# Optimization experiments

Hardware: AMD Instinct MI355X
Metric: run time of the kernel (lower is better)

The kernel has to match this reference:

```python
import jax, jax.numpy as jnp
import numpy as np

N, E = 32768, 262144
IN_C, OUT_C = 128, 128
N_GRAPHS = 64


def setup_inputs() -> dict:
    key = jax.random.key(0)
    ks = jax.random.split(key, 8)
    x = jax.random.normal(ks[0], (N, IN_C), dtype=jnp.float32)
    edge_index = jax.random.randint(ks[1], (2, E), 0, N, dtype=jnp.int32)
    batch = jnp.sort(jax.random.randint(ks[2], (N,), 0, N_GRAPHS, dtype=jnp.int32))
    rand = jax.random.uniform(ks[3], (E,), dtype=jnp.float32)  # replaces random.random() draws
    lim_t = 1.0 / np.sqrt(IN_C)
    W_t = jax.random.uniform(ks[4], (IN_C, OUT_C), jnp.float32, -lim_t, lim_t)
    b_t = jax.random.uniform(ks[5], (OUT_C,), jnp.float32, -lim_t, lim_t)
    lim_s = 1.0 / np.sqrt(OUT_C)
    W_s = jax.random.uniform(ks[6], (OUT_C, 1), jnp.float32, -lim_s, lim_s)
    b_s = jax.random.uniform(ks[7], (1,), jnp.float32, -lim_s, lim_s)
    return dict(x=x, edge_index=edge_index, batch=batch, rand=rand,
                W_t=W_t, b_t=b_t, W_s=W_s, b_s=b_s)


def _greedy_match(scores, src, dst, rand, n):
    """Sequential greedy edge matching over score-sorted edges.
    Returns (order, cid_sorted, n_merged): cid_sorted[i] is the cluster id
    assigned to sorted edge i, or -1 if rejected/skipped."""
    scores = jax.lax.stop_gradient(scores)  # indices are non-differentiable (torch uses .item())
    rand = jax.lax.stop_gradient(rand)
    order = jnp.argsort(-scores)
    s_o, d_o = src[order], dst[order]
    acc = rand[order] <= scores[order]  # torch: skip edge if r > edge_score

    def step(carry, inp):
        avail, nxt = carry
        s, t, a = inp
        ok = a & avail[s] & avail[t]
        cid = jnp.where(ok, nxt, -1)
        avail = avail.at[s].set(avail[s] & ~ok)
        avail = avail.at[t].set(avail[t] & ~ok)
        return (avail, nxt + ok.astype(jnp.int32)), cid

    (_, n_merged), cid_sorted = jax.lax.scan(
        step, (jnp.ones((n,), bool), jnp.int32(0)), (s_o, d_o, acc))
    return order, cid_sorted, n_merged


def reference(x, edge_index, batch, rand, W_t, b_t, W_s, b_s):
    n = x.shape[0]
    src, dst = edge_index[0], edge_index[1]
    # merge_edge_sum + transform (eval mode, dropout p=0)
    x_merged = (x[src] + x[dst]) @ W_t + b_t          # [E, OUT_C]
    x_self = (x + x) @ W_t + b_t                      # [N, OUT_C] (self-edge merge)
    e = jax.nn.sigmoid((x_merged @ W_s).reshape(-1) + b_s[0])  # [E] edge scores

    order, cid_sorted, n_merged = _greedy_match(e, src, dst, rand, n)
    ok = cid_sorted >= 0                              # accepted sorted edges
    s_o, d_o = src[order], dst[order]

    # node -> cluster assignment (sentinel index n is dropped)
    cluster = jnp.full((n,), -1, jnp.int32)
    cluster = cluster.at[jnp.where(ok, s_o, n)].set(cid_sorted, mode='drop')
    cluster = cluster.at[jnp.where(ok, d_o, n)].set(cid_sorted, mode='drop')
    remaining = cluster < 0
    rem_rank = jnp.cumsum(remaining.astype(jnp.int32)) - 1  # ascending node order, like set iteration
    cluster = jnp.where(remaining, n_merged + rem_rank, cluster)
    num_clusters = n_merged + remaining.sum().astype(jnp.int32)

    # pooled features, padded to [n, OUT_C]; rows [0, num_clusters) are valid
    mcid = jnp.where(ok, cid_sorted, n)
    new_x = jnp.zeros((n, x_merged.shape[1]), x.dtype)
    new_x = new_x.at[mcid].set(x_merged[order], mode='drop')
    new_x = new_x.at[jnp.where(remaining, cluster, n)].set(x_self, mode='drop')

    # per-cluster edge score (1.0 for unmerged singleton nodes)
    new_edge_score = jnp.ones((n,), e.dtype).at[mcid].set(e[order], mode='drop')

    # new batch vector: new_batch[cluster[v]] = batch[v]
    new_batch = jnp.zeros((n,), batch.dtype).at[cluster].set(batch)

    # remapped edges + coalesce/remove_self_loops expressed as a validity mask
    new_ei = cluster[edge_index]                      # [2, E]
    key = new_ei[0].astype(jnp.int64) * n + new_ei[1].astype(jnp.int64)
    perm = jnp.argsort(key)
    ksorted = key[perm]
    first = jnp.concatenate([jnp.array([True]), ksorted[1:] != ksorted[:-1]])
    unique = jnp.zeros((key.shape[0],), bool).at[perm].set(first)
    edge_valid = unique & (new_ei[0] != new_ei[1])

    return new_x, cluster, new_batch, new_edge_score, num_clusters, new_ei, edge_valid, e
```

## Files before the change

### kernel.cpp

```cpp
#include <hip/hip_runtime.h>
#include <stdint.h>

typedef unsigned int u32;
typedef unsigned long long u64;

#define NN 32768
#define NE 262144
#define NC 128

#define O0 0u
#define O1 4194304u
#define O2 4227072u
#define O3 4259840u
#define O4 4292608u
#define O5 4292609u
#define O6 4816897u
#define O7 5079041u

#define HCAP (1u<<19)
#define NFULL 8
#define CNT0 8
#define MCAP 16384
#define SCAP 32768
#define SNB 32
#define MAXK 0xFFFFFFFFFFFFFFFFull
#define PREFLAG (1ull<<62)

__global__ void ep_init(const float* Wt, const float* Ws, const float* bt, const float* bs,
                        double* u, double* c0, u32* counters,
                        u64* b0, u64* b1, u32* avail, int* cl,
                        u32* tkey, u32* tmin) {
    u32 i = blockIdx.x*blockDim.x + threadIdx.x;
    if (blockIdx.x == 0 && threadIdx.x < 128) {
        int r = threadIdx.x;
        double s = 0.0;
        for (int j = 0; j < NC; j++) s += (double)Wt[r*NC+j] * (double)Ws[j];
        u[r] = s;
        if (r == 0) {
            double c = 0.0;
            for (int j = 0; j < NC; j++) c += (double)bt[j] * (double)Ws[j];
            *c0 = c + (double)bs[0];
        }
    }
    if (i < 64) counters[i] = 0u;
    if (i < NN) { b0[i] = MAXK; b1[i] = MAXK; cl[i] = -1; }
    if (i < NN/32) avail[i] = 0xFFFFFFFFu;
    for (u32 j = i; j < HCAP; j += 131072u) { tkey[j] = 0xFFFFFFFFu; tmin[j] = 0xFFFFFFFFu; }
}

__global__ void ep_ynode(const float* x, const double* u, double* y) {
    int gid = blockIdx.x*blockDim.x + threadIdx.x;
    int v = gid >> 6, lane = threadIdx.x & 63;
    if (v >= NN) return;
    double t = (double)x[v*NC+lane]*u[lane] + (double)x[v*NC+lane+64]*u[lane+64];
    for (int off = 32; off; off >>= 1) t += __shfl_down(t, off, 64);
    if (lane == 0) y[v] = t;
}

__global__ void ep_escore(const int* src, const int* dst, const float* rnd, const double* y,
                          const double* c0, u64* fkey, u64* fdat, u32* counters, float* out) {
    int e = blockIdx.x*blockDim.x + threadIdx.x;
    if (e >= NE) return;
    int s = src[e], d = dst[e];
    double z = y[s] + y[d] + *c0;
    double sc = 1.0/(1.0 + exp(-z));
    out[O7 + e] = (float)sc;
    u64 b = (u64)__double_as_longlong(z);
    u64 ord = (b & 0x8000000000000000ull) ? ~b : (b | 0x8000000000000000ull);
    u64 P = ((~ord) & 0xFFFFFFFFFFFC0000ull) | (u64)(u32)e;
    if ((double)rnd[e] <= sc) {
        u32 p = atomicAdd(&counters[CNT0], 1u);
        fkey[p] = P;
        fdat[p] = ((u64)(u32)e << 30) | ((u64)(u32)s << 15) | (u64)(u32)d;
    }
}

__device__ __forceinline__ bool ep_bit(const u32* a, u32 v) { return (a[v>>5] >> (v&31)) & 1u; }

__global__ void ep_rA(const u64* fkey, const u64* fdat, const u32* cnt, u64* bt, const u32* avail) {
    u32 n = *cnt;
    for (u32 i = blockIdx.x*blockDim.x + threadIdx.x; i < n; i += 131072u) {
        u64 v = fdat[i];
        u32 s = (u32)((v>>15)&0x7FFF), d = (u32)(v&0x7FFF);
        if (ep_bit(avail, s) && ep_bit(avail, d)) {
            u64 P = fkey[i];
            atomicMin(&bt[s], P); atomicMin(&bt[d], P);
        }
    }
}

__global__ void ep_rB(const u64* fkey, const u64* fdat, const u32* cnt, u32* cntN,
                      u64* fkeyN, u64* fdatN, const u64* bt, u64* btN, u32* avail,
                      u64* mkey, u64* mpay, u32* counters) {
    u32 n = *cnt;
    for (u32 i = blockIdx.x*blockDim.x + threadIdx.x; i < n; i += 131072u) {
        u64 v = fdat[i];
        u32 s = (u32)((v>>15)&0x7FFF), d = (u32)(v&0x7FFF);
        if (!ep_bit(avail, s) || !ep_bit(avail, d)) continue;
        u64 P = fkey[i];
        if (bt[s] == P && bt[d] == P) {
            u32 slot = atomicAdd(&counters[2], 1u);
            mkey[slot] = P; mpay[slot] = v;
            atomicAnd(&avail[s>>5], ~(1u<<(s&31)));
            atomicAnd(&avail[d>>5], ~(1u<<(d&31)));
        } else {
            u32 p = atomicAdd(cntN, 1u);
            fkeyN[p] = P; fdatN[p] = v;
            btN[s] = MAXK; btN[d] = MAXK;
        }
    }
}

__global__ void ep_merge(const u64* mk, const u64* mp, const u64* fk, const u64* fd,
                         u32* counters, u64* ck, u64* cd2) {
    u32 i = blockIdx.x*blockDim.x + threadIdx.x;
    u32 nm0 = counters[2];
    u32 cr  = counters[CNT0+NFULL];
    if (i == 0) { u32 tot = nm0 + cr; counters[4] = tot > SCAP ? SCAP : tot; }
    u64 K = MAXK, D = 0;
    if (i < nm0) { K = mk[i]; D = mp[i] | PREFLAG; }
    else if (i < nm0 + cr && i < SCAP) { K = fk[i-nm0]; D = fd[i-nm0]; }
    ck[i] = K; cd2[i] = D;
}

__global__ void ms_hist(const u64* key, u32* hist, int shift) {
    __shared__ u32 h[256];
    int t = threadIdx.x;
    for (int i = t; i < 256; i += 64) h[i] = 0;
    __syncthreads();
    int base = blockIdx.x*1024 + t*16;
    for (int j = 0; j < 16; j++) {
        u32 dg = (u32)(key[base+j] >> shift) & 255u;
        atomicAdd(&h[dg], 1u);
    }
    __syncthreads();
    for (int i = t; i < 256; i += 64) hist[i*SNB + blockIdx.x] = h[i];
}

__global__ void ms_scan(u32* hist) {
    int t = threadIdx.x;
    int per = 256*SNB/64;
    int base = t*per;
    u32 s = 0;
    for (int j = 0; j < per; j++) s += hist[base+j];
    u32 x = s;
    for (int off = 1; off < 64; off <<= 1) { u32 yv = __shfl_up(x, off, 64); if (t >= off) x += yv; }
    u32 run = x - s;
    for (int j = 0; j < per; j++) { u32 tmp = hist[base+j]; hist[base+j] = run; run += tmp; }
}

__global__ void ms_scat(const u64* ki, const u64* pi, u64* ko, u64* po, const u32* hist, int shift) {
    __shared__ unsigned short m[256][64];
    int t = threadIdx.x;
    for (int i = t; i < 256*32; i += 64) ((u32*)m)[i] = 0u;
    __syncthreads();
    int base = blockIdx.x*1024 + t*16;
    u64 kr[16]; u32 dg[16];
    #pragma unroll
    for (int j = 0; j < 16; j++) {
        kr[j] = ki[base+j];
        dg[j] = (u32)(kr[j] >> shift) & 255u;
        m[dg[j]][t]++;
    }
    __syncthreads();
    for (int k = 0; k < 4; k++) {
        int d = t*4 + k;
        u32 run = 0;
        for (int tt = 0; tt < 64; tt++) { u32 tmp = m[d][tt]; m[d][tt] = (unsigned short)run; run += tmp; }
    }
    __syncthreads();
    #pragma unroll
    for (int j = 0; j < 16; j++) {
        u32 d = dg[j];
        u32 pos = hist[d*SNB + blockIdx.x] + m[d][t];
        m[d][t]++;
        ko[pos] = kr[j];
        po[pos] = pi[base+j];
    }
}

__global__ void ep_csum(const u64* sd, const u32* counters, u32* mflag, u32* csums) {
    u32 i = blockIdx.x*1024 + threadIdx.x;
    u32 cnt = counters[4];
    u64 v = sd[i];
    bool pre = (i < cnt) && ((v & PREFLAG) != 0);
    bool cand = (i < cnt) && !pre;
    mflag[i] = pre ? 1u : 0u;
    int c = __syncthreads_count(cand ? 1 : 0);
    if (threadIdx.x == 0) csums[blockIdx.x] = (u32)c;
}

__global__ void ep_cscan(u32* csums, u32* counters, int which) {
    int t = threadIdx.x;
    u32 v = (t < SNB) ? csums[t] : 0u;
    u32 x = v;
    for (int off = 1; off < 64; off <<= 1) { u32 y = __shfl_up(x, off, 64); if (t >= off) x += y; }
    if (t < SNB) csums[t] = x - v;
    if (t == SNB-1) counters[which] = x;
}

__global__ void ep_cemit(const u64* sd, const u32* counters, const u32* csums, u32* candIdx) {
    __shared__ u32 w[16];
    int t = threadIdx.x;
    u32 i = blockIdx.x*1024 + t;
    u32 cnt = counters[4];
    u64 v = sd[i];
    bool pre = (i < cnt) && ((v & PREFLAG) != 0);
    u32 c = ((i < cnt) && !pre) ? 1u : 0u;
    u32 x = c;
    for (int off = 1; off < 64; off <<= 1) { u32 y = __shfl_up(x, off, 64); if ((t&63) >= off) x += y; }
    if ((t&63) == 63) w[t>>6] = x;
    __syncthreads();
    if (t < 16) {
        u32 ww = w[t];
        for (int off = 1; off < 16; off <<= 1) { u32 y = __shfl_up(ww, off, 16); if (t >= off) ww += y; }
        w[t] = ww;
    }
    __syncthreads();
    u32 excl = ((t>>6) ? w[(t>>6)-1] : 0u) + x - c;
    if (c) candIdx[csums[blockIdx.x] + excl] = i;
}

__global__ void __launch_bounds__(1024) ep_walk(const u64* sd, const u32* candIdx,
                                                const u32* counters, const u32* availG,
                                                u32* mflag) {
    __shared__ u32 avail[1024];
    __shared__ u32 claim[16384];
    int t = threadIdx.x;
    avail[t] = availG[t];
    for (int j = t; j < 16384; j += 1024) claim[j] = 0xFFFFFFFFu;
    __syncthreads();
    u32 ncand = counters[5];
    for (u32 base = 0; base < ncand; base += 1024) {
        u32 j = base + t;
        bool have = j < ncand;
        u32 i = 0, s = 0, d = 0;
        if (have) {
            i = candIdx[j];
            u64 v = sd[i];
            s = (u32)((v>>15)&0x7FFF); d = (u32)(v&0x7FFF);
        }
        int st;
        if (!have) st = 1;
        else st = (((avail[s>>5]>>(s&31))&1u) && ((avail[d>>5]>>(d&31))&1u)) ? 0 : 1;
        for (int it = 0; __syncthreads_count(st == 0) > 0 && it < 300; it++) {
            u32 hs = s & 16383u, hd = d & 16383u;
            bool wrote = false;
            if (st == 0) { atomicMin(&claim[hs], (u32)t); atomicMin(&claim[hd], (u32)t); wrote = true; }
            __syncthreads();
            if (st == 0 && claim[hs] == (u32)t && claim[hd] == (u32)t) {
                st = 2;
                atomicAnd(&avail[s>>5], ~(1u<<(s&31)));
                atomicAnd(&avail[d>>5], ~(1u<<(d&31)));
            }
            __syncthreads();
            if (wrote) { claim[hs] = 0xFFFFFFFFu; claim[hd] = 0xFFFFFFFFu; }
            if (st == 0) {
                if (!((avail[s>>5]>>(s&31))&1u) || !((avail[d>>5]>>(d&31))&1u)) st = 1;
            }
        }
        if (st == 2) mflag[i] = 1u;
        __syncthreads();
    }
}

__global__ void ep_msum(const u32* mflag, u32* msums) {
    u32 i = blockIdx.x*1024 + threadIdx.x;
    int c = __syncthreads_count(mflag[i] != 0 ? 1 : 0);
    if (threadIdx.x == 0) msums[blockIdx.x] = (u32)c;
}

__global__ void ep_memit(const u64* sd, const u32* mflag, const u32* msums,
                         const int* batch, u64* Mlist, int* cl, float* out) {
    __shared__ u32 w[16];
    int t = threadIdx.x;
    u32 i = blockIdx.x*1024 + t;
    u32 m = mflag[i];
    u32 x = m;
    for (int off = 1; off < 64; off <<= 1) { u32 y = __shfl_up(x, off, 64); if ((t&63) >= off) x += y; }
    if ((t&63) == 63) w[t>>6] = x;
    __syncthreads();
    if (t < 16) {
        u32 ww = w[t];
        for (int off = 1; off < 16; off <<= 1) { u32 y = __shfl_up(ww, off, 16); if (t >= off) ww += y; }
        w[t] = ww;
    }
    __syncthreads();
    u32 excl = ((t>>6) ? w[(t>>6)-1] : 0u) + x - m;
    if (m) {
        u32 cid = msums[blockIdx.x] + excl;
        u64 v = sd[i] & ~PREFLAG;
        u32 e = (u32)(v>>30), s = (u32)((v>>15)&0x7FFF), d = (u32)(v&0x7FFF);
        Mlist[cid] = v;
        cl[s] = (int)cid; cl[d] = (int)cid;
        u32 mx = s > d ? s : d;
        out[O2 + cid] = (float)batch[mx];
        out[O3 + cid] = out[O7 + e];
    }
}

__global__ void ep_scanN(int* cl, u32* counters, u32* slist, float* out) {
    __shared__ u32 w[16];
    int t = threadIdx.x;
    int base = t*32;
    u32 s = 0;
    for (int j = 0; j < 32; j++) s += (cl[base+j] < 0) ? 1u : 0u;
    u32 x = s;
    for (int off = 1; off < 64; off <<= 1) { u32 y = __shfl_up(x, off, 64); if ((t&63) >= off) x += y; }
    if ((t&63) == 63) w[t>>6] = x;
    __syncthreads();
    if (t < 16) {
        u32 ww = w[t];
        for (int off = 1; off < 16; off <<= 1) { u32 y = __shfl_up(ww, off, 16); if (t >= off) ww += y; }
        w[t] = ww;
    }
    __syncthreads();
    u32 excl = ((t>>6) ? w[(t>>6)-1] : 0u) + x - s;
    u32 total = w[15];
    u32 nm = counters[2];
    if (t == 0) {
        counters[3] = nm + total;
        counters[6] = total;
        out[O4] = (float)(nm + total);
    }
    u32 run = nm + excl;
    for (int j = 0; j < 32; j++) {
        if (cl[base+j] < 0) {
            slist[run - nm] = (u32)(base + j);
            cl[base+j] = (int)(run++);
        }
    }
}

__global__ void ep_out_nodes(const int* cl, const int* batch, const u32* counters, float* out) {
    int v = blockIdx.x*blockDim.x + threadIdx.x;
    if (v >= NN) return;
    u32 nm = counters[2], ncl = counters[3];
    int c = cl[v];
    out[O1 + v] = (float)c;
    if (c >= (int)nm) out[O2 + c] = (float)batch[v];
    if (v >= (int)nm) out[O3 + v] = 1.0f;
    if (v >= (int)ncl) out[O2 + v] = 0.0f;
}

__global__ void ep_newx_m(const float* x, const float* Wt, const float* bt,
                          const u64* Mlist, const u32* counters, float* out) {
    __shared__ u64 ml[32];
    __shared__ float m[32][128];
    u32 nm = counters[2];
    u32 base = blockIdx.x * 32u;
    if (base >= nm) return;
    int t = threadIdx.x, lane = t & 63, wv = t >> 6;
    if (t < 32) { u32 r = base + (u32)t; ml[t] = (r < nm) ? Mlist[r] : 0ull; }
    __syncthreads();
    for (int i = t; i < 4096; i += 256) {
        int r = i >> 7, k = i & 127;
        u64 v = ml[r];
        u32 s = (u32)((v>>15)&0x7FFF), d = (u32)(v&0x7FFF);
        m[r][k] = x[s*NC+k] + x[d*NC+k];
    }
    __syncthreads();
    float a0[8], a1[8];
    #pragma unroll
    for (int r = 0; r < 8; r++) { a0[r] = bt[lane]; a1[r] = bt[lane+64]; }
    for (int k = 0; k < 128; k++) {
        float w0 = Wt[k*NC+lane], w1 = Wt[k*NC+lane+64];
        #pragma unroll
        for (int r = 0; r < 8; r++) { float mm = m[wv*8+r][k]; a0[r] += mm*w0; a1[r] += mm*w1; }
    }
    #pragma unroll
    for (int r = 0; r < 8; r++) {
        u32 row = base + (u32)(wv*8 + r);
        if (row < nm) {
            out[O0 + (size_t)row*NC + lane]      = a0[r];
            out[O0 + (size_t)row*NC + lane + 64] = a1[r];
        }
    }
}

__global__ void ep_newx_s(const float* x, const float* Wt, const float* bt,
                          const u32* slist, const u32* counters, float* out) {
    __shared__ u32 nodes[32];
    __shared__ float m[32][128];
    u32 nm = counters[2], ncl = counters[3], sc = counters[6];
    u32 base = nm + blockIdx.x * 32u;
    if (base >= NN) return;
    int t = threadIdx.x, lane = t & 63, wv = t >> 6;
    if (base >= ncl) {
        for (int i = t; i < 4096; i += 256) {
            u32 row = base + (u32)(i >> 7);
            if (row < NN) out[O0 + (size_t)row*NC + (i & 127)] = 0.0f;
        }
        return;
    }
    if (t < 32) { u32 p = base - nm + (u32)t; nodes[t] = (p < sc) ? slist[p] : slist[0]; }
    __syncthreads();
    for (int i = t; i < 4096; i += 256) {
        int r = i >> 7, k = i & 127;
        m[r][k] = 2.0f * x[nodes[r]*NC + k];
    }
    __syncthreads();
    float a0[8], a1[8];
    #pragma unroll
    for (int r = 0; r < 8; r++) { a0[r] = bt[lane]; a1[r] = bt[lane+64]; }
    for (int k = 0; k < 128; k++) {
        float w0 = Wt[k*NC+lane], w1 = Wt[k*NC+lane+64];
        #pragma unroll
        for (int r = 0; r < 8; r++) { float mm = m[wv*8+r][k]; a0[r] += mm*w0; a1[r] += mm*w1; }
    }
    #pragma unroll
    for (int r = 0; r < 8; r++) {
        u32 row = base + (u32)(wv*8 + r);
        if (row >= NN) continue;
        if (row < ncl) {
            out[O0 + (size_t)row*NC + lane]      = a0[r];
            out[O0 + (size_t)row*NC + lane + 64] = a1[r];
        } else {
            out[O0 + (size_t)row*NC + lane]      = 0.0f;
            out[O0 + (size_t)row*NC + lane + 64] = 0.0f;
        }
    }
}

__global__ void ep_newei(const int* src, const int* dst, const int* cl,
                         u32* tkey, u32* tmin, u32* eslot, float* out) {
    int e = blockIdx.x*blockDim.x + threadIdx.x;
    if (e >= NE) return;
    u32 cs = (u32)cl[src[e]], cd = (u32)cl[dst[e]];
    out[O5 + e]      = (float)cs;
    out[O5 + NE + e] = (float)cd;
    u32 key = (cs << 15) | cd;
    u32 slot = ((key * 2654435761u) >> 11) & (HCAP-1);
    while (true) {
        u32 k = tkey[slot];
        if (k == key) break;
        if (k == 0xFFFFFFFFu) {
            u32 old = atomicCAS(&tkey[slot], 0xFFFFFFFFu, key);
            if (old == 0xFFFFFFFFu || old == key) break;
        }
        slot = (slot + 1) & (HCAP-1);
    }
    eslot[e] = slot | ((cs != cd) ? 0x80000000u : 0u);
    atomicMin(&tmin[slot], (u32)e);
}

__global__ void ep_valid(const u32* tmin, const u32* eslot, float* out) {
    int e = blockIdx.x*blockDim.x + threadIdx.x;
    if (e >= NE) return;
    u32 sl = eslot[e];
    bool valid = (tmin[sl & 0x7FFFFFFFu] == (u32)e) && (sl >> 31);
    out[O6 + e] = valid ? 1.0f : 0.0f;
}

extern "C" void kernel_launch(void* const* d_in, const int* in_sizes, int n_in,
                              void* d_out, int out_size, void* d_ws, size_t ws_size,
                              hipStream_t stream) {
    (void)in_sizes; (void)n_in; (void)out_size; (void)ws_size;
    const float* x    = (const float*)d_in[0];
    const int*   ei   = (const int*)d_in[1];
    const int*   src  = ei;
    const int*   dst  = ei + NE;
    const int*   batch= (const int*)d_in[2];
    const float* rnd  = (const float*)d_in[3];
    const float* Wt   = (const float*)d_in[4];
    const float* bt   = (const float*)d_in[5];
    const float* Ws   = (const float*)d_in[6];
    const float* bs   = (const float*)d_in[7];
    float* out = (float*)d_out;

    char* w = (char*)d_ws;
    double* u  = (double*)w;
    double* c0 = (double*)(w + 1024);
    u32* counters = (u32*)(w + 2048);
    size_t off = 4096;
    double* y   = (double*)(w + off); off += (size_t)NN*8;
    u64* fkeyA  = (u64*)(w + off); off += (size_t)NE*8;
    u64* fdatA  = (u64*)(w + off); off += (size_t)NE*8;
    u64* fkeyB  = (u64*)(w + off); off += (size_t)NE*8;
    u64* fdatB  = (u64*)(w + off); off += (size_t)NE*8;
    u64* mkeyA  = (u64*)(w + off); off += (size_t)MCAP*8;
    u64* mpayA  = (u64*)(w + off); off += (size_t)MCAP*8;
    u64* combK  = (u64*)(w + off); off += (size_t)SCAP*8;
    u64* combD  = (u64*)(w + off); off += (size_t)SCAP*8;
    u64* combK2 = (u64*)(w + off); off += (size_t)SCAP*8;
    u64* combD2 = (u64*)(w + off); off += (size_t)SCAP*8;
    u64* bt0    = (u64*)(w + off); off += (size_t)NN*8;
    u64* bt1    = (u64*)(w + off); off += (size_t)NN*8;
    u32* avail  = (u32*)(w + off); off += NN/8;
    int* cl     = (int*)(w + off); off += (size_t)NN*4;
    u64* Mlist  = (u64*)(w + off); off += (size_t)NN*8;
    u32* hist   = (u32*)(w + off); off += 8192*4;
    u32* mflag  = (u32*)(w + off); off += (size_t)SCAP*4;
    u32* candIdx= (u32*)(w + off); off += (size_t)SCAP*4;
    u32* csums  = (u32*)(w + off); off += 64*4;
    u32* msums  = (u32*)(w + off); off += 64*4;
    u32* slist  = (u32*)(w + off); off += (size_t)NN*4;
    u32* tkey   = (u32*)(w + off); off += (size_t)HCAP*4;
    u32* tmin   = (u32*)(w + off); off += (size_t)HCAP*4;
    u32* eslot  = (u32*)(w + off); off += (size_t)NE*4;

    ep_init<<<512, 256, 0, stream>>>(Wt, Ws, bt, bs, u, c0, counters,
                                     bt0, bt1, avail, cl, tkey, tmin);
    ep_ynode<<<8192, 256, 0, stream>>>(x, u, y);
    ep_escore<<<1024, 256, 0, stream>>>(src, dst, rnd, y, c0, fkeyA, fdatA, counters, out);

    u64 *fk = fkeyA, *fd = fdatA, *fk2 = fkeyB, *fd2 = fdatB;
    u64 *bc = bt0, *bn = bt1;
    for (u32 rd = 0; rd < NFULL; rd++) {
        ep_rA<<<512, 256, 0, stream>>>(fk, fd, &counters[CNT0+rd], bc, avail);
        ep_rB<<<512, 256, 0, stream>>>(fk, fd, &counters[CNT0+rd], &counters[CNT0+rd+1],
                                       fk2, fd2, bc, bn, avail, mkeyA, mpayA, counters);
        u64* tp;
        tp = fk; fk = fk2; fk2 = tp;
        tp = fd; fd = fd2; fd2 = tp;
        tp = bc; bc = bn; bn = tp;
    }

    ep_merge<<<SNB, 1024, 0, stream>>>(mkeyA, mpayA, fk, fd, counters, combK, combD);
    u64 *ki = combK, *pi = combD, *ko = combK2, *po = combD2;
    for (int p = 0; p < 6; p++) {
        int shift = 16 + p*8;
        ms_hist<<<SNB, 64, 0, stream>>>(ki, hist, shift);
        ms_scan<<<1, 64, 0, stream>>>(hist);
        ms_scat<<<SNB, 64, 0, stream>>>(ki, pi, ko, po, hist, shift);
        u64* tp;
        tp = ki; ki = ko; ko = tp;
        tp = pi; pi = po; po = tp;
    }

    ep_csum<<<SNB, 1024, 0, stream>>>(combD, counters, mflag, csums);
    ep_cscan<<<1, 64, 0, stream>>>(csums, counters, 5);
    ep_cemit<<<SNB, 1024, 0, stream>>>(combD, counters, csums, candIdx);
    ep_walk<<<1, 1024, 0, stream>>>(combD, candIdx, counters, avail, mflag);
    ep_msum<<<SNB, 1024, 0, stream>>>(mflag, msums);
    ep_cscan<<<1, 64, 0, stream>>>(msums, counters, 2);
    ep_memit<<<SNB, 1024, 0, stream>>>(combD, mflag, msums, batch, Mlist, cl, out);

    ep_scanN<<<1, 1024, 0, stream>>>(cl, counters, slist, out);
    ep_out_nodes<<<128, 256, 0, stream>>>(cl, batch, counters, out);

    ep_newx_m<<<512, 256, 0, stream>>>(x, Wt, bt, Mlist, counters, out);
    ep_newx_s<<<1024, 256, 0, stream>>>(x, Wt, bt, slist, counters, out);

    ep_newei<<<1024, 256, 0, stream>>>(src, dst, cl, tkey, tmin, eslot, out);
    ep_valid<<<1024, 256, 0, stream>>>(tmin, eslot, out);
}
```

Before: 650.0 us.

## Run conflict-resolution walk in one wavefront and fold match count into it

The sequential greedy walk over candidate edges now runs in a single 64-lane wavefront. It uses __any instead of block-wide __syncthreads_count barriers, and the claim hash table shrinks to 4096 entries. The walk kernel also computes the per-segment merged counts and the total, which removes the separate ep_msum and ep_cscan launches. The radix sort passes now skip loads and stores beyond the live element count. In exchange, each batch resolves only 64 candidates instead of 1024, and the smaller hash gives more false conflicts between unrelated nodes.

```diff
diff --git a/kernel.cpp b/kernel.cpp
--- a/kernel.cpp
+++ b/kernel.cpp
@@ -123,14 +123,16 @@
     ck[i] = K; cd2[i] = D;
 }
 
-__global__ void ms_hist(const u64* key, u32* hist, int shift) {
+__global__ void ms_hist(const u64* key, u32* hist, int shift, const u32* counters) {
     __shared__ u32 h[256];
     int t = threadIdx.x;
+    u32 cnt = counters[4];
     for (int i = t; i < 256; i += 64) h[i] = 0;
     __syncthreads();
-    int base = blockIdx.x*1024 + t*16;
-    for (int j = 0; j < 16; j++) {
-        u32 dg = (u32)(key[base+j] >> shift) & 255u;
+    u32 base = blockIdx.x*1024u + (u32)t*16u;
+    for (u32 j = 0; j < 16; j++) {
+        u64 k = (base+j < cnt) ? key[base+j] : MAXK;
+        u32 dg = (u32)(k >> shift) & 255u;
         atomicAdd(&h[dg], 1u);
     }
     __syncthreads();
@@ -149,16 +151,18 @@
     for (int j = 0; j < per; j++) { u32 tmp = hist[base+j]; hist[base+j] = run; run += tmp; }
 }
 
-__global__ void ms_scat(const u64* ki, const u64* pi, u64* ko, u64* po, const u32* hist, int shift) {
+__global__ void ms_scat(const u64* ki, const u64* pi, u64* ko, u64* po,
+                        const u32* hist, int shift, const u32* counters) {
     __shared__ unsigned short m[256][64];
     int t = threadIdx.x;
+    u32 cnt = counters[4];
     for (int i = t; i < 256*32; i += 64) ((u32*)m)[i] = 0u;
     __syncthreads();
-    int base = blockIdx.x*1024 + t*16;
+    u32 base = blockIdx.x*1024u + (u32)t*16u;
     u64 kr[16]; u32 dg[16];
     #pragma unroll
-    for (int j = 0; j < 16; j++) {
-        kr[j] = ki[base+j];
+    for (u32 j = 0; j < 16; j++) {
+        kr[j] = (base+j < cnt) ? ki[base+j] : MAXK;
         dg[j] = (u32)(kr[j] >> shift) & 255u;
         m[dg[j]][t]++;
     }
@@ -170,12 +174,14 @@
     }
     __syncthreads();
     #pragma unroll
-    for (int j = 0; j < 16; j++) {
+    for (u32 j = 0; j < 16; j++) {
         u32 d = dg[j];
         u32 pos = hist[d*SNB + blockIdx.x] + m[d][t];
         m[d][t]++;
-        ko[pos] = kr[j];
-        po[pos] = pi[base+j];
+        if (base+j < cnt) {
+            ko[pos] = kr[j];
+            po[pos] = pi[base+j];
+        }
     }
 }
 
@@ -222,52 +228,55 @@
 }
 
 __global__ void __launch_bounds__(1024) ep_walk(const u64* sd, const u32* candIdx,
-                                                const u32* counters, const u32* availG,
-                                                u32* mflag) {
+                                                u32* counters, const u32* availG,
+                                                u32* mflag, u32* msums) {
     __shared__ u32 avail[1024];
-    __shared__ u32 claim[16384];
+    __shared__ u32 claim[4096];
+    __shared__ u32 part[1024];
+    __shared__ u32 segs[32];
     int t = threadIdx.x;
     avail[t] = availG[t];
-    for (int j = t; j < 16384; j += 1024) claim[j] = 0xFFFFFFFFu;
-    __syncthreads();
-    u32 ncand = counters[5];
-    for (u32 base = 0; base < ncand; base += 1024) {
-        u32 j = base + t;
-        bool have = j < ncand;
-        u32 i = 0, s = 0, d = 0;
-        if (have) {
-            i = candIdx[j];
-            u64 v = sd[i];
-            s = (u32)((v>>15)&0x7FFF); d = (u32)(v&0x7FFF);
-        }
-        int st;
-        if (!have) st = 1;
-        else st = (((avail[s>>5]>>(s&31))&1u) && ((avail[d>>5]>>(d&31))&1u)) ? 0 : 1;
-        for (int it = 0; __syncthreads_count(st == 0) > 0 && it < 300; it++) {
-            u32 hs = s & 16383u, hd = d & 16383u;
-            bool wrote = false;
-            if (st == 0) { atomicMin(&claim[hs], (u32)t); atomicMin(&claim[hd], (u32)t); wrote = true; }
-            __syncthreads();
-            if (st == 0 && claim[hs] == (u32)t && claim[hd] == (u32)t) {
-                st = 2;
-                atomicAnd(&avail[s>>5], ~(1u<<(s&31)));
-                atomicAnd(&avail[d>>5], ~(1u<<(d&31)));
+    for (int j = t; j < 4096; j += 1024) claim[j] = 0xFFFFFFFFu;
+    __syncthreads();
+    if (t < 64) {
+        int lane = t;
+        u32 ncand = counters[5];
+        for (u32 base = 0; base < ncand; base += 64) {
+            u32 j = base + (u32)lane;
+            u32 i = 0, s = 0, d = 0;
+            int st = 1;
+            if (j < ncand) {
+                i = candIdx[j];
+                u64 v = sd[i];
+                s = (u32)((v>>15)&0x7FFF); d = (u32)(v&0x7FFF);
+                st = (((avail[s>>5]>>(s&31))&1u) && ((avail[d>>5]>>(d&31))&1u)) ? 0 : 1;
             }
-            __syncthreads();
-            if (wrote) { claim[hs] = 0xFFFFFFFFu; claim[hd] = 0xFFFFFFFFu; }
-            if (st == 0) {
-                if (!((avail[s>>5]>>(s&31))&1u) || !((avail[d>>5]>>(d&31))&1u)) st = 1;
+            u32 hs = s & 4095u, hd = d & 4095u;
+            int guard = 0;
+            while (__any(st == 0) && guard++ < 80) {
+                if (st == 0) { atomicMin(&claim[hs], (u32)lane); atomicMin(&claim[hd], (u32)lane); }
+                bool win = (st == 0) && (claim[hs] == (u32)lane) && (claim[hd] == (u32)lane);
+                if (win) {
+                    st = 2;
+                    atomicAnd(&avail[s>>5], ~(1u<<(s&31)));
+                    atomicAnd(&avail[d>>5], ~(1u<<(d&31)));
+                    mflag[i] = 1u;
+                }
+                if (st == 0 || win) { claim[hs] = 0xFFFFFFFFu; claim[hd] = 0xFFFFFFFFu; }
+                if (st == 0) {
+                    if (!(((avail[s>>5]>>(s&31))&1u) && ((avail[d>>5]>>(d&31))&1u))) st = 1;
+                }
             }
         }
-        if (st == 2) mflag[i] = 1u;
-        __syncthreads();
-    }
-}
-
-__global__ void ep_msum(const u32* mflag, u32* msums) {
-    u32 i = blockIdx.x*1024 + threadIdx.x;
-    int c = __syncthreads_count(mflag[i] != 0 ? 1 : 0);
-    if (threadIdx.x == 0) msums[blockIdx.x] = (u32)c;
+    }
+    __syncthreads();
+    u32 p = 0; int b2 = t*32;
+    for (int j = 0; j < 32; j++) p += mflag[b2+j];
+    part[t] = p;
+    __syncthreads();
+    if (t < 32) { u32 sg = 0; for (int j = 0; j < 32; j++) sg += part[t*32+j]; segs[t] = sg; }
+    __syncthreads();
+    if (t == 0) { u32 a = 0; for (int g = 0; g < 32; g++) { msums[g] = a; a += segs[g]; } counters[2] = a; }
 }
 
 __global__ void ep_memit(const u64* sd, const u32* mflag, const u32* msums,
@@ -520,9 +529,9 @@
     u64 *ki = combK, *pi = combD, *ko = combK2, *po = combD2;
     for (int p = 0; p < 6; p++) {
         int shift = 16 + p*8;
-        ms_hist<<<SNB, 64, 0, stream>>>(ki, hist, shift);
+        ms_hist<<<SNB, 64, 0, stream>>>(ki, hist, shift, counters);
         ms_scan<<<1, 64, 0, stream>>>(hist);
-        ms_scat<<<SNB, 64, 0, stream>>>(ki, pi, ko, po, hist, shift);
+        ms_scat<<<SNB, 64, 0, stream>>>(ki, pi, ko, po, hist, shift, counters);
         u64* tp;
         tp = ki; ki = ko; ko = tp;
         tp = pi; pi = po; po = tp;
@@ -531,9 +540,7 @@
     ep_csum<<<SNB, 1024, 0, stream>>>(combD, counters, mflag, csums);
     ep_cscan<<<1, 64, 0, stream>>>(csums, counters, 5);
     ep_cemit<<<SNB, 1024, 0, stream>>>(combD, counters, csums, candIdx);
-    ep_walk<<<1, 1024, 0, stream>>>(combD, candIdx, counters, avail, mflag);
-    ep_msum<<<SNB, 1024, 0, stream>>>(mflag, msums);
-    ep_cscan<<<1, 64, 0, stream>>>(msums, counters, 2);
+    ep_walk<<<1, 1024, 0, stream>>>(combD, candIdx, counters, avail, mflag, msums);
     ep_memit<<<SNB, 1024, 0, stream>>>(combD, mflag, msums, batch, Mlist, cl, out);
 
     ep_scanN<<<1, 1024, 0, stream>>>(cl, counters, slist, out);
```

Measured after the change: 866.9 us. +33.4%, slower.
